# Performance work log

Hardware: AMD Instinct MI355X
Metric: run time of the kernel (lower is better)

Reference implementation:

```python
import jax, jax.numpy as jnp
import numpy as np

# torch grid_sample semantics: grid[...,0] indexes width, grid[...,1] height, grid[...,2] depth;
# align_corners=True -> idx = (g+1)/2*(size-1); padding_mode='zeros' -> out-of-range taps contribute 0.

def _bilinear(plane, gx, gy):
    # plane: (C,H,W); gx,gy: (P,) in [-1,1]. Returns (P,C).
    C, H, W = plane.shape
    ix = (gx + 1.0) * 0.5 * (W - 1)
    iy = (gy + 1.0) * 0.5 * (H - 1)
    x0 = jnp.floor(ix); y0 = jnp.floor(iy)
    wx = ix - x0; wy = iy - y0
    x0i = x0.astype(jnp.int32); x1i = x0i + 1
    y0i = y0.astype(jnp.int32); y1i = y0i + 1
    def tap(xi, yi):
        valid = ((xi >= 0) & (xi < W) & (yi >= 0) & (yi < H)).astype(plane.dtype)
        v = plane[:, jnp.clip(yi, 0, H - 1), jnp.clip(xi, 0, W - 1)]  # (C,P)
        return v * valid
    out = (tap(x0i, y0i) * ((1 - wx) * (1 - wy)) + tap(x1i, y0i) * (wx * (1 - wy))
         + tap(x0i, y1i) * ((1 - wx) * wy)      + tap(x1i, y1i) * (wx * wy))
    return out.T  # (P,C)


def _trilinear(vol, gx, gy, gz):
    # vol: (C,D,H,W); gx->W, gy->H, gz->D. Returns (P,C).
    C, D, H, W = vol.shape
    ix = (gx + 1.0) * 0.5 * (W - 1)
    iy = (gy + 1.0) * 0.5 * (H - 1)
    iz = (gz + 1.0) * 0.5 * (D - 1)
    x0 = jnp.floor(ix); y0 = jnp.floor(iy); z0 = jnp.floor(iz)
    wx = ix - x0; wy = iy - y0; wz = iz - z0
    x0i = x0.astype(jnp.int32); y0i = y0.astype(jnp.int32); z0i = z0.astype(jnp.int32)
    def tap(xi, yi, zi):
        valid = ((xi >= 0) & (xi < W) & (yi >= 0) & (yi < H) & (zi >= 0) & (zi < D)).astype(vol.dtype)
        v = vol[:, jnp.clip(zi, 0, D - 1), jnp.clip(yi, 0, H - 1), jnp.clip(xi, 0, W - 1)]
        return v * valid
    out = jnp.zeros((C, gx.shape[0]), vol.dtype)
    for dz, wz_ in ((0, 1 - wz), (1, wz)):
        for dy, wy_ in ((0, 1 - wy), (1, wy)):
            for dx, wx_ in ((0, 1 - wx), (1, wx)):
                out = out + tap(x0i + dx, y0i + dy, z0i + dz) * (wx_ * wy_ * wz_)
    return out.T


def setup_inputs() -> dict:
    key = jax.random.key(0)
    ks = jax.random.split(key, 16)
    P, Cp, Np_, Cl, Nl, Cv, Nv = 262144, 32, 128, 64, 128, 16, 64
    s = 0.001
    d = {
        'coordinates': jax.random.uniform(ks[0], (1, P, 3), jnp.float32, -1.0, 1.0),
        'plane_xy': jax.random.normal(ks[1], (Cp, Np_, Np_)) * s,
        'plane_yz': jax.random.normal(ks[2], (Cp, Np_, Np_)) * s,
        'plane_xz': jax.random.normal(ks[3], (Cp, Np_, Np_)) * s,
        'plane_xy_g': jax.random.normal(ks[4], (Cp, Np_, Np_)) * s,
        'plane_yz_g': jax.random.normal(ks[5], (Cp, Np_, Np_)) * s,
        'plane_xz_g': jax.random.normal(ks[6], (Cp, Np_, Np_)) * s,
        'line_x': jax.random.normal(ks[7], (Cl, Nl, 1)) * s,
        'line_y': jax.random.normal(ks[8], (Cl, Nl, 1)) * s,
        'line_z': jax.random.normal(ks[9], (Cl, Nl, 1)) * s,
        'line_x_g': jax.random.normal(ks[10], (Cl, Nl, 1)) * s,
        'line_y_g': jax.random.normal(ks[11], (Cl, Nl, 1)) * s,
        'line_z_g': jax.random.normal(ks[12], (Cl, Nl, 1)) * s,
        'volume': jax.random.normal(ks[13], (Cv, Nv, Nv, Nv)) * s,
        'volume_g': jax.random.normal(ks[14], (Cv, Nv, Nv, Nv)) * s,
    }
    return d


def reference(coordinates, plane_xy, plane_yz, plane_xz, plane_xy_g, plane_yz_g, plane_xz_g,
              line_x, line_y, line_z, line_x_g, line_y_g, line_z_g, volume, volume_g):
    c = coordinates[0]  # (P,3), batch squeezed as in torch .squeeze(0)
    x, y, z = c[:, 0], c[:, 1], c[:, 2]
    zero = jnp.zeros_like(x)
    # Planes: coords2d (a,b) -> grid x=a (width), grid y=b (height).
    xy_e = _bilinear(plane_xy, x, y); xy_g = _bilinear(plane_xy_g, x, y)
    yz_e = _bilinear(plane_yz, y, z); yz_g = _bilinear(plane_yz_g, y, z)
    xz_e = _bilinear(plane_xz, x, z); xz_g = _bilinear(plane_xz_g, x, z)
    feats = jnp.sum(xy_e * (xy_g >= 0) + yz_e * (yz_g >= 0) + xz_e * (xz_g >= 0), axis=-1)
    # Lines: grid pair is (coord, 0) -> coord indexes the singleton width dim (faithful to torch).
    x_e = _bilinear(line_x, x, zero); x_g = _bilinear(line_x_g, x, zero)
    y_e = _bilinear(line_y, y, zero); y_g = _bilinear(line_y_g, y, zero)
    z_e = _bilinear(line_z, z, zero); z_g = _bilinear(line_z_g, z, zero)
    line_feats = jnp.sum(x_e * (x_g >= 0) + y_e * (y_g >= 0) + z_e * (z_g >= 0), axis=-1)
    # Volume: grid (x,y,z) -> x:W, y:H, z:D.
    v_e = _trilinear(volume, x, y, z); v_g = _trilinear(volume_g, x, y, z)
    vol_feats = jnp.sum(v_e * (v_g >= 0), axis=-1)
    return feats + line_feats + vol_feats  # (P,)
```

## Files before the change

kernel.cpp:

```cpp
#include <hip/hip_runtime.h>
#include <hip/hip_bf16.h>

#pragma clang fp contract(off)

typedef unsigned short u16;
typedef unsigned int u32;
typedef __attribute__((ext_vector_type(4))) float f32x4;
typedef __attribute__((ext_vector_type(8))) unsigned short u16x8;
typedef __attribute__((ext_vector_type(4))) unsigned short u16x4;

__device__ __forceinline__ float bf2f(u16 u) {
    union { unsigned int i; float f; } v; v.i = ((unsigned int)u) << 16; return v.f;
}
__device__ __forceinline__ u16 f2bf(float f) {
    __hip_bfloat16 h = __float2bfloat16(f);
    return *(u16*)&h;
}

__device__ __forceinline__ int cell_of(float x, float y, float z)
{
    int cx = (int)fminf(fmaxf((x + 1.0f) * 4.0f, 0.0f), 7.0f);
    int cy = (int)fminf(fmaxf((y + 1.0f) * 4.0f, 0.0f), 7.0f);
    int cz = (int)fminf(fmaxf((z + 1.0f) * 4.0f, 0.0f), 7.0f);
    return cx + (cy << 3) + (cz << 6);
}

__global__ __launch_bounds__(256) void fused_prep_count(
    const float* __restrict__ pxy, const float* __restrict__ pxyg,
    const float* __restrict__ pyz, const float* __restrict__ pyzg,
    const float* __restrict__ pxz, const float* __restrict__ pxzg,
    const float* __restrict__ vol, const float* __restrict__ volg,
    char* __restrict__ tpxy, char* __restrict__ tpyz, char* __restrict__ tpxz,
    char* __restrict__ tv,
    const float* __restrict__ coords, u32* __restrict__ hist, int P)
{
    __shared__ float smem[4352];
    const int b = blockIdx.x;
    const int t = threadIdx.x;

    if (b < 768) {
        int which = b >> 8, blk = b & 255;
        const float* e = (which == 0) ? pxy  : (which == 1) ? pyz  : pxz;
        const float* g = (which == 0) ? pxyg : (which == 1) ? pyzg : pxzg;
        char* dst      = (which == 0) ? tpxy : (which == 1) ? tpyz : tpxz;
        const int tbase = blk * 64;
#pragma unroll
        for (int i = 0; i < 4; ++i) {
            int eidx = i * 256 + t;
            int c = eidx >> 4;
            int q = eidx & 15;
            const float* src = (c < 32) ? e : g;
            int cs = (c < 32) ? c : (c - 32);
            f32x4 v = *(const f32x4*)(src + (size_t)cs * 16384 + tbase + q * 4);
            *(f32x4*)&smem[c * 68 + q * 4] = v;
        }
        __syncthreads();
#pragma unroll
        for (int i = 0; i < 3; ++i) {
            int sid = i * 256 + t;
            int rec = sid / 12;
            int seg = sid % 12;
            char* outp = dst + (size_t)(tbase + rec) * 192 + seg * 16;
            if (seg < 4) {
                u16x8 pk;
#pragma unroll
                for (int k = 0; k < 8; ++k) pk[k] = f2bf(smem[(seg * 8 + k) * 68 + rec]);
                *(u16x8*)outp = pk;
            } else {
                f32x4 pk;
#pragma unroll
                for (int k = 0; k < 4; ++k) pk[k] = smem[(32 + (seg - 4) * 4 + k) * 68 + rec];
                *(f32x4*)outp = pk;
            }
        }
    } else if (b < 2816) {
        int blk = b - 768;
        const int tbase = blk * 128;
#pragma unroll
        for (int i = 0; i < 4; ++i) {
            int eidx = i * 256 + t;
            int c = eidx >> 5;
            int q = eidx & 31;
            const float* src = (c < 16) ? vol : volg;
            int cs = (c < 16) ? c : (c - 16);
            f32x4 v = *(const f32x4*)(src + (size_t)cs * 262144 + tbase + q * 4);
            *(f32x4*)&smem[c * 132 + q * 4] = v;
        }
        __syncthreads();
#pragma unroll
        for (int i = 0; i < 3; ++i) {
            int sid = i * 256 + t;
            int rec = sid / 6;
            int seg = sid % 6;
            char* outp = tv + (size_t)(tbase + rec) * 96 + seg * 16;
            if (seg < 2) {
                u16x8 pk;
#pragma unroll
                for (int k = 0; k < 8; ++k) pk[k] = f2bf(smem[(seg * 8 + k) * 132 + rec]);
                *(u16x8*)outp = pk;
            } else {
                f32x4 pk;
#pragma unroll
                for (int k = 0; k < 4; ++k) pk[k] = smem[(16 + (seg - 2) * 4 + k) * 132 + rec];
                *(f32x4*)outp = pk;
            }
        }
    } else {
        u32* h = (u32*)smem;
        int blk = b - 2816;
        h[t] = 0u; h[t + 256] = 0u;
        __syncthreads();
#pragma unroll
        for (int i = 0; i < 4; ++i) {
            int p = blk * 1024 + i * 256 + t;
            if (p < P) {
                float x = coords[3 * p + 0];
                float y = coords[3 * p + 1];
                float z = coords[3 * p + 2];
                atomicAdd(&h[cell_of(x, y, z)], 1u);
            }
        }
        __syncthreads();
        u32* hb = hist + (size_t)blk * 512;
        hb[t] = h[t];
        hb[t + 256] = h[t + 256];
    }
}

__global__ __launch_bounds__(256) void cell_base(
    const u32* __restrict__ hist, u32* __restrict__ base,
    u32* __restrict__ totals, float* __restrict__ lcout,
    const float* __restrict__ lx,  const float* __restrict__ ly,  const float* __restrict__ lz,
    const float* __restrict__ lxg, const float* __restrict__ lyg, const float* __restrict__ lzg,
    int nb)
{
    int c = blockIdx.x;
    int t = threadIdx.x;
    u32 v = (t < nb) ? hist[(size_t)t * 512 + c] : 0u;
    __shared__ u32 ls[256];
    ls[t] = v;
    __syncthreads();
#pragma unroll
    for (int off = 1; off < 256; off <<= 1) {
        u32 x = (t >= off) ? ls[t - off] : 0u;
        __syncthreads();
        ls[t] += x;
        __syncthreads();
    }
    if (t < nb) base[(size_t)t * 512 + c] = ls[t] - v;
    if (t == 255) totals[c] = ls[255];

    if (c == 0 && t < 64) {
        float ev, gv, part = 0.0f;
        ev = lx[t * 128 + 63] * 0.5f + lx[t * 128 + 64] * 0.5f;
        gv = lxg[t * 128 + 63] * 0.5f + lxg[t * 128 + 64] * 0.5f;
        part += (gv >= 0.0f) ? ev : 0.0f;
        ev = ly[t * 128 + 63] * 0.5f + ly[t * 128 + 64] * 0.5f;
        gv = lyg[t * 128 + 63] * 0.5f + lyg[t * 128 + 64] * 0.5f;
        part += (gv >= 0.0f) ? ev : 0.0f;
        ev = lz[t * 128 + 63] * 0.5f + lz[t * 128 + 64] * 0.5f;
        gv = lzg[t * 128 + 63] * 0.5f + lzg[t * 128 + 64] * 0.5f;
        part += (gv >= 0.0f) ? ev : 0.0f;
#pragma unroll
        for (int off = 32; off > 0; off >>= 1) part += __shfl_down(part, off);
        if (t == 0) lcout[0] = part;
    }
}

__global__ __launch_bounds__(256) void scatter_sorted(
    const float* __restrict__ coords, const u32* __restrict__ base,
    const u32* __restrict__ totals, f32x4* __restrict__ sorted, int P)
{
    __shared__ u32 lh[512];
    __shared__ u32 ts[512];
    __shared__ u32 torig[512];
    int t = threadIdx.x;
    lh[t] = 0u; lh[t + 256] = 0u;
    u32 a0 = totals[t], a1 = totals[t + 256];
    ts[t] = a0; ts[t + 256] = a1;
    torig[t] = a0; torig[t + 256] = a1;
    __syncthreads();
#pragma unroll
    for (int off = 1; off < 512; off <<= 1) {
        u32 x0 = (t >= off) ? ts[t - off] : 0u;
        u32 x1 = (t + 256 >= off) ? ts[t + 256 - off] : 0u;
        __syncthreads();
        ts[t] += x0; ts[t + 256] += x1;
        __syncthreads();
    }
    ts[t]       -= torig[t];
    ts[t + 256] -= torig[t + 256];
    __syncthreads();

    int blk = blockIdx.x;
#pragma unroll
    for (int i = 0; i < 4; ++i) {
        int p = blk * 1024 + i * 256 + t;
        if (p < P) {
            float x = coords[3 * p + 0];
            float y = coords[3 * p + 1];
            float z = coords[3 * p + 2];
            int cell = cell_of(x, y, z);
            u32 rank = atomicAdd(&lh[cell], 1u);
            u32 pos = ts[cell] + base[(size_t)blk * 512 + cell] + rank;
            f32x4 v = {x, y, z, __uint_as_float((u32)p)};
            sorted[pos] = v;
        }
    }
}

__device__ __forceinline__ float plane_lane(
    const char* __restrict__ tp, float gx, float gy, int s)
{
    float ix = fminf(fmaxf((gx + 1.0f) * 0.5f * 127.0f, 0.0f), 127.0f);
    float iy = fminf(fmaxf((gy + 1.0f) * 0.5f * 127.0f, 0.0f), 127.0f);
    float x0f = floorf(ix), y0f = floorf(iy);
    float wx = ix - x0f, wy = iy - y0f;
    int x0 = (int)x0f, y0 = (int)y0f;
    int x1 = x0 + 1, y1 = y0 + 1;
    float vx1 = (x1 < 128) ? 1.0f : 0.0f;
    float vy1 = (y1 < 128) ? 1.0f : 0.0f;
    int x1c = min(x1, 127), y1c = min(y1, 127);
    float omwx = 1.0f - wx, omwy = 1.0f - wy;
    float ws4[4];
    ws4[0] = omwx * omwy;
    ws4[1] = (wx * omwy) * vx1;
    ws4[2] = (omwx * wy) * vy1;
    ws4[3] = ((wx * wy) * vx1) * vy1;
    unsigned o[4];
    o[0] = (unsigned)(y0  * 128 + x0 ) * 192u;
    o[1] = (unsigned)(y0  * 128 + x1c) * 192u;
    o[2] = (unsigned)(y1c * 128 + x0 ) * 192u;
    o[3] = (unsigned)(y1c * 128 + x1c) * 192u;

    const int eoff = s * 16;
    const int goff = 64 + s * 32;
    f32x4 ea0 = {0.0f, 0.0f, 0.0f, 0.0f}, ea1 = {0.0f, 0.0f, 0.0f, 0.0f};
    f32x4 ga0 = {0.0f, 0.0f, 0.0f, 0.0f}, ga1 = {0.0f, 0.0f, 0.0f, 0.0f};
#pragma unroll
    for (int t = 0; t < 4; ++t) {
        const char* bp = tp + o[t];
        float w = ws4[t];
        u16x8 ev = *(const u16x8*)(bp + eoff);
        f32x4 g0 = *(const f32x4*)(bp + goff);
        f32x4 g1 = *(const f32x4*)(bp + goff + 16);
#pragma unroll
        for (int j = 0; j < 4; ++j) {
            ga0[j] = ga0[j] + g0[j] * w;
            ga1[j] = ga1[j] + g1[j] * w;
            ea0[j] = fmaf(bf2f(ev[j]), w, ea0[j]);
            ea1[j] = fmaf(bf2f(ev[j + 4]), w, ea1[j]);
        }
    }
    float acc = 0.0f;
#pragma unroll
    for (int j = 0; j < 4; ++j) {
        acc += (ga0[j] >= 0.0f) ? ea0[j] : 0.0f;
        acc += (ga1[j] >= 0.0f) ? ea1[j] : 0.0f;
    }
    return acc;
}

__device__ __forceinline__ float vol_lane(
    const char* __restrict__ tv, float gx, float gy, float gz, int s)
{
    float ix = fminf(fmaxf((gx + 1.0f) * 0.5f * 63.0f, 0.0f), 63.0f);
    float iy = fminf(fmaxf((gy + 1.0f) * 0.5f * 63.0f, 0.0f), 63.0f);
    float iz = fminf(fmaxf((gz + 1.0f) * 0.5f * 63.0f, 0.0f), 63.0f);
    float x0f = floorf(ix), y0f = floorf(iy), z0f = floorf(iz);
    float wx = ix - x0f, wy = iy - y0f, wz = iz - z0f;
    int x0 = (int)x0f, y0 = (int)y0f, z0 = (int)z0f;
    int x1 = x0 + 1, y1 = y0 + 1, z1 = z0 + 1;
    float fx[2] = {1.0f - wx, wx}, fy[2] = {1.0f - wy, wy}, fz[2] = {1.0f - wz, wz};
    float vx[2] = {1.0f, (x1 < 64) ? 1.0f : 0.0f};
    float vy[2] = {1.0f, (y1 < 64) ? 1.0f : 0.0f};
    float vz[2] = {1.0f, (z1 < 64) ? 1.0f : 0.0f};
    int xi[2] = {x0, min(x1, 63)}, yi[2] = {y0, min(y1, 63)}, zi[2] = {z0, min(z1, 63)};

    unsigned off[8];
    float w[8];
#pragma unroll
    for (int dz = 0; dz < 2; ++dz)
#pragma unroll
        for (int dy = 0; dy < 2; ++dy)
#pragma unroll
            for (int dx = 0; dx < 2; ++dx) {
                int tt = (dz << 2) | (dy << 1) | dx;
                w[tt] = (((fx[dx] * fy[dy]) * fz[dz]) * vx[dx]) * (vy[dy] * vz[dz]);
                off[tt] = (unsigned)((zi[dz] * 64 + yi[dy]) * 64 + xi[dx]) * 96u;
            }
    const int eoff = s * 8;
    const int goff = 32 + s * 16;
    f32x4 ea = {0.0f, 0.0f, 0.0f, 0.0f}, ga = {0.0f, 0.0f, 0.0f, 0.0f};
#pragma unroll
    for (int tt = 0; tt < 8; ++tt) {
        const char* bp = tv + off[tt];
        float wt = w[tt];
        u16x4 ev = *(const u16x4*)(bp + eoff);
        f32x4 gv = *(const f32x4*)(bp + goff);
#pragma unroll
        for (int j = 0; j < 4; ++j) {
            ga[j] = ga[j] + gv[j] * wt;
            ea[j] = fmaf(bf2f(ev[j]), wt, ea[j]);
        }
    }
    float acc = 0.0f;
#pragma unroll
    for (int j = 0; j < 4; ++j)
        acc += (ga[j] >= 0.0f) ? ea[j] : 0.0f;
    return acc;
}

__global__ __launch_bounds__(256) void ctri_main_S2(
    const f32x4* __restrict__ sorted, const float* __restrict__ lcbuf,
    const char* __restrict__ tpxy, const char* __restrict__ tpyz, const char* __restrict__ tpxz,
    const char* __restrict__ tv,
    float* __restrict__ out, int P, int nblk)
{
    float lc = lcbuf[0];
    int b = blockIdx.x;
    int cpx = nblk >> 3;
    int swz = (b & 7) * cpx + (b >> 3);
    int g = threadIdx.x >> 2;
    int s = threadIdx.x & 3;
    int i0 = swz * 128 + g * 2;
    if (i0 >= P) return;
    int i1 = min(i0 + 1, P - 1);
    f32x4 s0 = sorted[i0];
    f32x4 s1 = sorted[i1];
    int p0 = (int)__float_as_uint(s0[3]);
    int p1 = (int)__float_as_uint(s1[3]);
    float a0 = 0.0f, a1 = 0.0f;
    a0 += plane_lane(tpxy, s0[0], s0[1], s);    a1 += plane_lane(tpxy, s1[0], s1[1], s);
    a0 += plane_lane(tpyz, s0[1], s0[2], s);    a1 += plane_lane(tpyz, s1[1], s1[2], s);
    a0 += plane_lane(tpxz, s0[0], s0[2], s);    a1 += plane_lane(tpxz, s1[0], s1[2], s);
    a0 += vol_lane(tv, s0[0], s0[1], s0[2], s); a1 += vol_lane(tv, s1[0], s1[1], s1[2], s);
    a0 += __shfl_xor(a0, 1, 64);
    a0 += __shfl_xor(a0, 2, 64);
    a1 += __shfl_xor(a1, 1, 64);
    a1 += __shfl_xor(a1, 2, 64);
    if (s == 0) {
        out[p0] = lc + a0;
        if (i0 + 1 < P) out[p1] = lc + a1;
    }
}

__device__ __forceinline__ float line_pair(const float* __restrict__ e,
                                           const float* __restrict__ g, int c)
{
    float ev = e[c * 128 + 63] * 0.5f + e[c * 128 + 64] * 0.5f;
    float gv = g[c * 128 + 63] * 0.5f + g[c * 128 + 64] * 0.5f;
    return (gv >= 0.0f) ? ev : 0.0f;
}

__device__ __forceinline__ float block_line_const(
    const float* lx, const float* ly, const float* lz,
    const float* lxg, const float* lyg, const float* lzg)
{
    __shared__ float lc_sh;
    int t = threadIdx.x;
    if (t < 64) {
        float part = line_pair(lx, lxg, t) + line_pair(ly, lyg, t) + line_pair(lz, lzg, t);
#pragma unroll
        for (int off = 32; off > 0; off >>= 1) part += __shfl_down(part, off);
        if (t == 0) lc_sh = part;
    }
    __syncthreads();
    return lc_sh;
}

__device__ __forceinline__ float sample_plane_pair_D(
    const float* __restrict__ e, const float* __restrict__ g, float gx, float gy)
{
    float ix = fminf(fmaxf((gx + 1.0f) * 0.5f * 127.0f, 0.0f), 127.0f);
    float iy = fminf(fmaxf((gy + 1.0f) * 0.5f * 127.0f, 0.0f), 127.0f);
    float x0f = floorf(ix), y0f = floorf(iy);
    float wx = ix - x0f, wy = iy - y0f;
    int x0 = (int)x0f, y0 = (int)y0f;
    int x1 = x0 + 1, y1 = y0 + 1;
    float vx1 = (x1 < 128) ? 1.0f : 0.0f;
    float vy1 = (y1 < 128) ? 1.0f : 0.0f;
    int x1c = min(x1, 127), y1c = min(y1, 127);
    float omwx = 1.0f - wx, omwy = 1.0f - wy;
    float w00 = omwx * omwy;
    float w10 = (wx * omwy) * vx1;
    float w01 = (omwx * wy) * vy1;
    float w11 = ((wx * wy) * vx1) * vy1;
    int o00 = y0 * 128 + x0, o10 = y0 * 128 + x1c;
    int o01 = y1c * 128 + x0, o11 = y1c * 128 + x1c;
    float acc = 0.0f;
#pragma unroll 4
    for (int c = 0; c < 32; ++c) {
        const float* ec = e + (size_t)c * 16384;
        const float* gc = g + (size_t)c * 16384;
        float ei = ((ec[o00] * w00 + ec[o10] * w10) + ec[o01] * w01) + ec[o11] * w11;
        float gi = ((gc[o00] * w00 + gc[o10] * w10) + gc[o01] * w01) + gc[o11] * w11;
        acc += (gi >= 0.0f) ? ei : 0.0f;
    }
    return acc;
}

__device__ __forceinline__ float sample_volume_D(
    const float* __restrict__ e, const float* __restrict__ g,
    float gx, float gy, float gz)
{
    float ix = fminf(fmaxf((gx + 1.0f) * 0.5f * 63.0f, 0.0f), 63.0f);
    float iy = fminf(fmaxf((gy + 1.0f) * 0.5f * 63.0f, 0.0f), 63.0f);
    float iz = fminf(fmaxf((gz + 1.0f) * 0.5f * 63.0f, 0.0f), 63.0f);
    float x0f = floorf(ix), y0f = floorf(iy), z0f = floorf(iz);
    float wx = ix - x0f, wy = iy - y0f, wz = iz - z0f;
    int x0 = (int)x0f, y0 = (int)y0f, z0 = (int)z0f;
    int x1 = x0 + 1, y1 = y0 + 1, z1 = z0 + 1;
    float fx[2] = {1.0f - wx, wx}, fy[2] = {1.0f - wy, wy}, fz[2] = {1.0f - wz, wz};
    float vx[2] = {1.0f, (x1 < 64) ? 1.0f : 0.0f};
    float vy[2] = {1.0f, (y1 < 64) ? 1.0f : 0.0f};
    float vz[2] = {1.0f, (z1 < 64) ? 1.0f : 0.0f};
    int xi[2] = {x0, min(x1, 63)}, yi[2] = {y0, min(y1, 63)}, zi[2] = {z0, min(z1, 63)};
    int o[8]; float w[8];
#pragma unroll
    for (int dz = 0; dz < 2; ++dz)
#pragma unroll
        for (int dy = 0; dy < 2; ++dy)
#pragma unroll
            for (int dx = 0; dx < 2; ++dx) {
                int tt = (dz << 2) | (dy << 1) | dx;
                w[tt] = (((fx[dx] * fy[dy]) * fz[dz]) * vx[dx]) * (vy[dy] * vz[dz]);
                o[tt] = (zi[dz] * 64 + yi[dy]) * 64 + xi[dx];
            }
    float acc = 0.0f;
#pragma unroll 2
    for (int c = 0; c < 16; ++c) {
        const float* ec = e + (size_t)c * 262144;
        const float* gc = g + (size_t)c * 262144;
        float ei = 0.0f, gi = 0.0f;
#pragma unroll
        for (int tt = 0; tt < 8; ++tt) {
            ei = ei + ec[o[tt]] * w[tt];
            gi = gi + gc[o[tt]] * w[tt];
        }
        acc += (gi >= 0.0f) ? ei : 0.0f;
    }
    return acc;
}

__global__ __launch_bounds__(256) void ctri_main_D(
    const float* __restrict__ coords,
    const float* __restrict__ lx,  const float* __restrict__ ly,  const float* __restrict__ lz,
    const float* __restrict__ lxg, const float* __restrict__ lyg, const float* __restrict__ lzg,
    const float* __restrict__ pxy, const float* __restrict__ pyz, const float* __restrict__ pxz,
    const float* __restrict__ pxyg, const float* __restrict__ pyzg, const float* __restrict__ pxzg,
    const float* __restrict__ vol, const float* __restrict__ volg,
    float* __restrict__ out, int P)
{
    float lc = block_line_const(lx, ly, lz, lxg, lyg, lzg);
    int p = blockIdx.x * blockDim.x + threadIdx.x;
    if (p >= P) return;
    float x = coords[3 * p + 0];
    float y = coords[3 * p + 1];
    float z = coords[3 * p + 2];
    float acc = lc;
    acc += sample_plane_pair_D(pxy, pxyg, x, y);
    acc += sample_plane_pair_D(pyz, pyzg, y, z);
    acc += sample_plane_pair_D(pxz, pxzg, x, z);
    acc += sample_volume_D(vol, volg, x, y, z);
    out[p] = acc;
}

extern "C" void kernel_launch(void* const* d_in, const int* in_sizes, int n_in,
                              void* d_out, int out_size, void* d_ws, size_t ws_size,
                              hipStream_t stream)
{
    (void)n_in; (void)out_size;
    const float* coords = (const float*)d_in[0];
    const float* pxy  = (const float*)d_in[1];
    const float* pyz  = (const float*)d_in[2];
    const float* pxz  = (const float*)d_in[3];
    const float* pxyg = (const float*)d_in[4];
    const float* pyzg = (const float*)d_in[5];
    const float* pxzg = (const float*)d_in[6];
    const float* lx   = (const float*)d_in[7];
    const float* ly   = (const float*)d_in[8];
    const float* lz   = (const float*)d_in[9];
    const float* lxg  = (const float*)d_in[10];
    const float* lyg  = (const float*)d_in[11];
    const float* lzg  = (const float*)d_in[12];
    const float* vol  = (const float*)d_in[13];
    const float* volg = (const float*)d_in[14];
    float* out = (float*)d_out;

    const int P = in_sizes[0] / 3;
    const int chunks = (P + 1023) / 1024;
    const size_t planeRec = (size_t)16384 * 192;
    const size_t volRec   = (size_t)262144 * 96;
    const size_t tabBytes = 3 * planeRec + volRec;
    const size_t sortBytes = (size_t)P * 16;
    const size_t histBytes = (size_t)chunks * 512 * 4;
    const size_t need_bytes = tabBytes + sortBytes + 2 * histBytes + 512 * 4 + 64;

    if (ws_size >= need_bytes) {
        char* tpxy = (char*)d_ws;
        char* tpyz = tpxy + planeRec;
        char* tpxz = tpyz + planeRec;
        char* tv   = tpxz + planeRec;
        f32x4* sorted = (f32x4*)(tv + volRec);
        u32* hist   = (u32*)(sorted + P);
        u32* base   = hist + (size_t)chunks * 512;
        u32* totals = base + (size_t)chunks * 512;
        float* lcbuf = (float*)(totals + 512);

        fused_prep_count<<<2816 + chunks, 256, 0, stream>>>(
            pxy, pxyg, pyz, pyzg, pxz, pxzg, vol, volg,
            tpxy, tpyz, tpxz, tv, coords, hist, P);
        cell_base<<<512, 256, 0, stream>>>(hist, base, totals, lcbuf,
                                           lx, ly, lz, lxg, lyg, lzg, chunks);
        scatter_sorted<<<chunks, 256, 0, stream>>>(coords, base, totals, sorted, P);

        const int mblocks = (P * 2 + 255) / 256;
        ctri_main_S2<<<mblocks, 256, 0, stream>>>(sorted, lcbuf,
                                                  tpxy, tpyz, tpxz, tv, out, P, mblocks);
    } else {
        const int pblocks = (P + 255) / 256;
        ctri_main_D<<<pblocks, 256, 0, stream>>>(coords, lx, ly, lz, lxg, lyg, lzg,
                                                 pxy, pyz, pxz, pxyg, pyzg, pxzg,
                                                 vol, volg, out, P);
    }
}
```

Baseline: 174.8 us.

## Drop cell_base kernel by folding per-chunk prefix into scatter and prep

```diff
diff --git a/kernel.cpp b/kernel.cpp
--- a/kernel.cpp
+++ b/kernel.cpp
@@ -8,6 +8,8 @@
 typedef __attribute__((ext_vector_type(4))) float f32x4;
 typedef __attribute__((ext_vector_type(8))) unsigned short u16x8;
 typedef __attribute__((ext_vector_type(4))) unsigned short u16x4;
+typedef __attribute__((ext_vector_type(4))) unsigned int u32x4;
+typedef __attribute__((ext_vector_type(2))) unsigned int u32x2;
 
 __device__ __forceinline__ float bf2f(u16 u) {
     union { unsigned int i; float f; } v; v.i = ((unsigned int)u) << 16; return v.f;
@@ -15,6 +17,12 @@
 __device__ __forceinline__ u16 f2bf(float f) {
     __hip_bfloat16 h = __float2bfloat16(f);
     return *(u16*)&h;
+}
+__device__ __forceinline__ float bflo(u32 w) {
+    union { unsigned int i; float f; } v; v.i = w << 16; return v.f;
+}
+__device__ __forceinline__ float bfhi(u32 w) {
+    union { unsigned int i; float f; } v; v.i = w & 0xffff0000u; return v.f;
 }
 
 __device__ __forceinline__ int cell_of(float x, float y, float z)
@@ -32,7 +40,11 @@
     const float* __restrict__ vol, const float* __restrict__ volg,
     char* __restrict__ tpxy, char* __restrict__ tpyz, char* __restrict__ tpxz,
     char* __restrict__ tv,
-    const float* __restrict__ coords, u32* __restrict__ hist, int P)
+    const float* __restrict__ coords, u32* __restrict__ hist,
+    float* __restrict__ lcout,
+    const float* __restrict__ lx,  const float* __restrict__ ly,  const float* __restrict__ lz,
+    const float* __restrict__ lxg, const float* __restrict__ lyg, const float* __restrict__ lzg,
+    int P)
 {
     __shared__ float smem[4352];
     const int b = blockIdx.x;
@@ -73,6 +85,21 @@
                 *(f32x4*)outp = pk;
             }
         }
+        if (b == 0 && t < 64) {
+            float ev, gv, part = 0.0f;
+            ev = lx[t * 128 + 63] * 0.5f + lx[t * 128 + 64] * 0.5f;
+            gv = lxg[t * 128 + 63] * 0.5f + lxg[t * 128 + 64] * 0.5f;
+            part += (gv >= 0.0f) ? ev : 0.0f;
+            ev = ly[t * 128 + 63] * 0.5f + ly[t * 128 + 64] * 0.5f;
+            gv = lyg[t * 128 + 63] * 0.5f + lyg[t * 128 + 64] * 0.5f;
+            part += (gv >= 0.0f) ? ev : 0.0f;
+            ev = lz[t * 128 + 63] * 0.5f + lz[t * 128 + 64] * 0.5f;
+            gv = lzg[t * 128 + 63] * 0.5f + lzg[t * 128 + 64] * 0.5f;
+            part += (gv >= 0.0f) ? ev : 0.0f;
+#pragma unroll
+            for (int off = 32; off > 0; off >>= 1) part += __shfl_down(part, off);
+            if (t == 0) lcout[0] = part;
+        }
     } else if (b < 2816) {
         int blk = b - 768;
         const int tbase = blk * 128;
@@ -127,58 +154,26 @@
     }
 }
 
-__global__ __launch_bounds__(256) void cell_base(
-    const u32* __restrict__ hist, u32* __restrict__ base,
-    u32* __restrict__ totals, float* __restrict__ lcout,
-    const float* __restrict__ lx,  const float* __restrict__ ly,  const float* __restrict__ lz,
-    const float* __restrict__ lxg, const float* __restrict__ lyg, const float* __restrict__ lzg,
-    int nb)
-{
-    int c = blockIdx.x;
-    int t = threadIdx.x;
-    u32 v = (t < nb) ? hist[(size_t)t * 512 + c] : 0u;
-    __shared__ u32 ls[256];
-    ls[t] = v;
-    __syncthreads();
-#pragma unroll
-    for (int off = 1; off < 256; off <<= 1) {
-        u32 x = (t >= off) ? ls[t - off] : 0u;
-        __syncthreads();
-        ls[t] += x;
-        __syncthreads();
-    }
-    if (t < nb) base[(size_t)t * 512 + c] = ls[t] - v;
-    if (t == 255) totals[c] = ls[255];
-
-    if (c == 0 && t < 64) {
-        float ev, gv, part = 0.0f;
-        ev = lx[t * 128 + 63] * 0.5f + lx[t * 128 + 64] * 0.5f;
-        gv = lxg[t * 128 + 63] * 0.5f + lxg[t * 128 + 64] * 0.5f;
-        part += (gv >= 0.0f) ? ev : 0.0f;
-        ev = ly[t * 128 + 63] * 0.5f + ly[t * 128 + 64] * 0.5f;
-        gv = lyg[t * 128 + 63] * 0.5f + lyg[t * 128 + 64] * 0.5f;
-        part += (gv >= 0.0f) ? ev : 0.0f;
-        ev = lz[t * 128 + 63] * 0.5f + lz[t * 128 + 64] * 0.5f;
-        gv = lzg[t * 128 + 63] * 0.5f + lzg[t * 128 + 64] * 0.5f;
-        part += (gv >= 0.0f) ? ev : 0.0f;
-#pragma unroll
-        for (int off = 32; off > 0; off >>= 1) part += __shfl_down(part, off);
-        if (t == 0) lcout[0] = part;
-    }
-}
-
-__global__ __launch_bounds__(256) void scatter_sorted(
-    const float* __restrict__ coords, const u32* __restrict__ base,
-    const u32* __restrict__ totals, f32x4* __restrict__ sorted, int P)
+__global__ __launch_bounds__(256) void scatter_sorted2(
+    const float* __restrict__ coords, const u32* __restrict__ hist,
+    f32x4* __restrict__ sorted, int P, int nb)
 {
     __shared__ u32 lh[512];
     __shared__ u32 ts[512];
-    __shared__ u32 torig[512];
+    __shared__ u32 st[512];
     int t = threadIdx.x;
+    int b = blockIdx.x;
+
+    u32 my0 = 0, my1 = 0, tot0 = 0, tot1 = 0;
+#pragma unroll 8
+    for (int bb = 0; bb < nb; ++bb) {
+        u32 v0 = hist[(size_t)bb * 512 + t];
+        u32 v1 = hist[(size_t)bb * 512 + t + 256];
+        tot0 += v0; tot1 += v1;
+        if (bb < b) { my0 += v0; my1 += v1; }
+    }
     lh[t] = 0u; lh[t + 256] = 0u;
-    u32 a0 = totals[t], a1 = totals[t + 256];
-    ts[t] = a0; ts[t + 256] = a1;
-    torig[t] = a0; torig[t + 256] = a1;
+    ts[t] = tot0; ts[t + 256] = tot1;
     __syncthreads();
 #pragma unroll
     for (int off = 1; off < 512; off <<= 1) {
@@ -188,21 +183,20 @@
         ts[t] += x0; ts[t + 256] += x1;
         __syncthreads();
     }
-    ts[t]       -= torig[t];
-    ts[t + 256] -= torig[t + 256];
+    st[t]       = ts[t]       - tot0 + my0;
+    st[t + 256] = ts[t + 256] - tot1 + my1;
     __syncthreads();
 
-    int blk = blockIdx.x;
 #pragma unroll
     for (int i = 0; i < 4; ++i) {
-        int p = blk * 1024 + i * 256 + t;
+        int p = b * 1024 + i * 256 + t;
         if (p < P) {
             float x = coords[3 * p + 0];
             float y = coords[3 * p + 1];
             float z = coords[3 * p + 2];
             int cell = cell_of(x, y, z);
             u32 rank = atomicAdd(&lh[cell], 1u);
-            u32 pos = ts[cell] + base[(size_t)blk * 512 + cell] + rank;
+            u32 pos = st[cell] + rank;
             f32x4 v = {x, y, z, __uint_as_float((u32)p)};
             sorted[pos] = v;
         }
@@ -241,16 +235,22 @@
     for (int t = 0; t < 4; ++t) {
         const char* bp = tp + o[t];
         float w = ws4[t];
-        u16x8 ev = *(const u16x8*)(bp + eoff);
+        u32x4 ev = *(const u32x4*)(bp + eoff);
         f32x4 g0 = *(const f32x4*)(bp + goff);
         f32x4 g1 = *(const f32x4*)(bp + goff + 16);
 #pragma unroll
         for (int j = 0; j < 4; ++j) {
             ga0[j] = ga0[j] + g0[j] * w;
             ga1[j] = ga1[j] + g1[j] * w;
-            ea0[j] = fmaf(bf2f(ev[j]), w, ea0[j]);
-            ea1[j] = fmaf(bf2f(ev[j + 4]), w, ea1[j]);
-        }
+        }
+        ea0[0] = fmaf(bflo(ev[0]), w, ea0[0]);
+        ea0[1] = fmaf(bfhi(ev[0]), w, ea0[1]);
+        ea0[2] = fmaf(bflo(ev[1]), w, ea0[2]);
+        ea0[3] = fmaf(bfhi(ev[1]), w, ea0[3]);
+        ea1[0] = fmaf(bflo(ev[2]), w, ea1[0]);
+        ea1[1] = fmaf(bfhi(ev[2]), w, ea1[1]);
+        ea1[2] = fmaf(bflo(ev[3]), w, ea1[2]);
+        ea1[3] = fmaf(bfhi(ev[3]), w, ea1[3]);
     }
     float acc = 0.0f;
 #pragma unroll
@@ -296,13 +296,15 @@
     for (int tt = 0; tt < 8; ++tt) {
         const char* bp = tv + off[tt];
         float wt = w[tt];
-        u16x4 ev = *(const u16x4*)(bp + eoff);
+        u32x2 ev = *(const u32x2*)(bp + eoff);
         f32x4 gv = *(const f32x4*)(bp + goff);
 #pragma unroll
-        for (int j = 0; j < 4; ++j) {
+        for (int j = 0; j < 4; ++j)
             ga[j] = ga[j] + gv[j] * wt;
-            ea[j] = fmaf(bf2f(ev[j]), wt, ea[j]);
-        }
+        ea[0] = fmaf(bflo(ev[0]), wt, ea[0]);
+        ea[1] = fmaf(bfhi(ev[0]), wt, ea[1]);
+        ea[2] = fmaf(bflo(ev[1]), wt, ea[2]);
+        ea[3] = fmaf(bfhi(ev[1]), wt, ea[3]);
     }
     float acc = 0.0f;
 #pragma unroll
@@ -495,7 +497,7 @@
     const size_t tabBytes = 3 * planeRec + volRec;
     const size_t sortBytes = (size_t)P * 16;
     const size_t histBytes = (size_t)chunks * 512 * 4;
-    const size_t need_bytes = tabBytes + sortBytes + 2 * histBytes + 512 * 4 + 64;
+    const size_t need_bytes = tabBytes + sortBytes + histBytes + 64;
 
     if (ws_size >= need_bytes) {
         char* tpxy = (char*)d_ws;
@@ -503,17 +505,14 @@
         char* tpxz = tpyz + planeRec;
         char* tv   = tpxz + planeRec;
         f32x4* sorted = (f32x4*)(tv + volRec);
-        u32* hist   = (u32*)(sorted + P);
-        u32* base   = hist + (size_t)chunks * 512;
-        u32* totals = base + (size_t)chunks * 512;
-        float* lcbuf = (float*)(totals + 512);
+        u32* hist    = (u32*)(sorted + P);
+        float* lcbuf = (float*)(hist + (size_t)chunks * 512);
 
         fused_prep_count<<<2816 + chunks, 256, 0, stream>>>(
             pxy, pxyg, pyz, pyzg, pxz, pxzg, vol, volg,
-            tpxy, tpyz, tpxz, tv, coords, hist, P);
-        cell_base<<<512, 256, 0, stream>>>(hist, base, totals, lcbuf,
-                                           lx, ly, lz, lxg, lyg, lzg, chunks);
-        scatter_sorted<<<chunks, 256, 0, stream>>>(coords, base, totals, sorted, P);
+            tpxy, tpyz, tpxz, tv, coords, hist, lcbuf,
+            lx, ly, lz, lxg, lyg, lzg, P);
+        scatter_sorted2<<<chunks, 256, 0, stream>>>(coords, hist, sorted, P, chunks);
 
         const int mblocks = (P * 2 + 255) / 256;
         ctri_main_S2<<<mblocks, 256, 0, stream>>>(sorted, lcbuf,
```

Result: slower. 178.9 us (+2.3%).
